# Kernel tuning notes

Measured on AMD Instinct MI355X. Metric: run time of the kernel, lower is better.

## Reference

```python
import jax, jax.numpy as jnp
import numpy as np

N = 50000      # nodes
E = 800000     # edges (avg degree 16)
IN, HID, OUT = 128, 128, 64


def setup_inputs() -> dict:
    key = jax.random.key(0)
    ks = jax.random.split(key, 6)
    x = jax.random.normal(ks[0], (N, IN), dtype=jnp.float32)
    edge_index = jax.random.randint(ks[1], (2, E), 0, N, dtype=jnp.int32)
    # GCNConv params (glorot-ish scaling)
    W1 = jax.random.normal(ks[2], (IN, HID), dtype=jnp.float32) * (1.0 / np.sqrt(IN))
    b1 = jnp.zeros((HID,), dtype=jnp.float32)
    W2 = jax.random.normal(ks[3], (HID, OUT), dtype=jnp.float32) * (1.0 / np.sqrt(HID))
    b2 = jnp.zeros((OUT,), dtype=jnp.float32)
    return {"x": x, "edge_index": edge_index, "W1": W1, "b1": b1, "W2": W2, "b2": b2}


def _gcn_conv(h, edge_index, W, b):
    """PyG GCNConv: linear transform, then sym-normalized aggregation with self-loops."""
    h = h @ W  # [N, out]
    src, dst = edge_index[0], edge_index[1]
    # degree including the added self-loop
    deg = jax.ops.segment_sum(jnp.ones((E,), h.dtype), dst, num_segments=N) + 1.0
    dinv = jax.lax.rsqrt(deg)                       # deg^{-1/2}
    norm = dinv[src] * dinv[dst]                    # [E]
    agg = jax.ops.segment_sum(h[src] * norm[:, None], dst, num_segments=N)
    agg = agg + h * (dinv * dinv)[:, None]          # self-loop term: deg^{-1} * h_i
    return agg + b


def reference(x, edge_index, W1, b1, W2, b2):
    h = jax.nn.relu(_gcn_conv(x, edge_index, W1, b1))
    h = jax.nn.relu(_gcn_conv(h, edge_index, W2, b2))
    return h
```

## Files before the change

### kernel.cpp

```cpp
#include <hip/hip_runtime.h>

#define DIN 128
#define DHID 128
#define DOUT 64
#define CAPB 6144
#define CHUNK 4096
#define EPT (CHUNK / 256)

typedef short bf16x8 __attribute__((ext_vector_type(8)));
typedef float f32x4 __attribute__((ext_vector_type(4)));

static __device__ __forceinline__ unsigned short f2bf(float f) {
  union { float f; unsigned u; } v; v.f = f;
  unsigned r = v.u + 0x7fffu + ((v.u >> 16) & 1u);
  return (unsigned short)(r >> 16);
}
static __device__ __forceinline__ float bf_lo(unsigned v) {
  union { unsigned u; float f; } t; t.u = v << 16; return t.f;
}
static __device__ __forceinline__ float bf_hi(unsigned v) {
  union { unsigned u; float f; } t; t.u = v & 0xffff0000u; return t.f;
}

static __device__ __forceinline__ void wcast_body(
    const float* __restrict__ W, unsigned short* __restrict__ Wf,
    int NOUT, int tid) {
  int f = tid >> 6;
  int lane = tid & 63;
  int t = f & 3;
  int nt = f >> 2;
  int kbase = t * 32 + (lane >> 4) * 8;
  int n = nt * 16 + (lane & 15);
#pragma unroll
  for (int j = 0; j < 8; ++j)
    Wf[(size_t)tid * 8 + j] = f2bf(W[(size_t)(kbase + j) * NOUT + n]);
}

__global__ __launch_bounds__(256) void init_kernel(
    const float* __restrict__ W1, const float* __restrict__ W2,
    unsigned short* __restrict__ Wf1, unsigned short* __restrict__ Wf2,
    int* __restrict__ bincursor) {
  const int b = blockIdx.x;
  const int t = threadIdx.x;
  if (b == 0) {
    bincursor[t] = 0;
  } else if (b <= 8) {
    wcast_body(W1, Wf1, DHID, (b - 1) * 256 + t);
  } else {
    wcast_body(W2, Wf2, DOUT, (b - 9) * 256 + t);
  }
}

static __device__ void gemm1_tile(
    const float* __restrict__ A, const unsigned short* __restrict__ Wf,
    unsigned short* __restrict__ C, int M, int tile) {
  constexpr int NT = DHID / 16;
  const int lane = threadIdx.x & 63;
  const int wave = threadIdx.x >> 6;
  const int g = lane >> 4;
  const int m15 = lane & 15;

  bf16x8 bfrag[NT * 4];
#pragma unroll
  for (int f = 0; f < NT * 4; ++f)
    bfrag[f] = *(const bf16x8*)(Wf + ((size_t)(f * 64 + lane)) * 8);

  const int rowbase = tile * 64 + wave * 16;
  if (rowbase >= M) return;
  f32x4 acc[NT];
#pragma unroll
  for (int nt = 0; nt < NT; ++nt) acc[nt] = (f32x4){0.f, 0.f, 0.f, 0.f};
  const float* arow = A + (size_t)(rowbase + m15) * 128 + g * 8;
  bf16x8 af[4];
#pragma unroll
  for (int t = 0; t < 4; ++t) {
    float4 a0 = *(const float4*)(arow + t * 32);
    float4 a1 = *(const float4*)(arow + t * 32 + 4);
    bf16x8 f;
    f[0] = (short)f2bf(a0.x); f[1] = (short)f2bf(a0.y);
    f[2] = (short)f2bf(a0.z); f[3] = (short)f2bf(a0.w);
    f[4] = (short)f2bf(a1.x); f[5] = (short)f2bf(a1.y);
    f[6] = (short)f2bf(a1.z); f[7] = (short)f2bf(a1.w);
    af[t] = f;
  }
#pragma unroll
  for (int t = 0; t < 4; ++t)
#pragma unroll
    for (int nt = 0; nt < NT; ++nt)
      acc[nt] = __builtin_amdgcn_mfma_f32_16x16x32_bf16(
          af[t], bfrag[nt * 4 + t], acc[nt], 0, 0, 0);
#pragma unroll
  for (int nt = 0; nt < NT; ++nt)
#pragma unroll
    for (int r = 0; r < 4; ++r) {
      int row = rowbase + g * 4 + r;
      if (row < M)
        C[(size_t)row * DHID + nt * 16 + m15] = f2bf(acc[nt][r]);
    }
}

__global__ __launch_bounds__(256) void phaseA_kernel(
    const int* __restrict__ src, const int* __restrict__ dst,
    int* __restrict__ bincursor, unsigned* __restrict__ binbuf, int E,
    int nbinA, const float* __restrict__ x,
    const unsigned short* __restrict__ Wf1, unsigned short* __restrict__ h1,
    int M) {
  __shared__ int hist[256];
  __shared__ int cnt[256];
  __shared__ int offs[256];
  __shared__ int cur[256];
  __shared__ int gbase[256];
  __shared__ unsigned stage[CHUNK];

  if ((int)blockIdx.x >= nbinA) {
    gemm1_tile(x, Wf1, h1, M, (int)blockIdx.x - nbinA);
    return;
  }

  const int t = threadIdx.x;
  const int base = blockIdx.x * CHUNK;
  const int n = min(CHUNK, E - base);

  hist[t] = 0;
  __syncthreads();

  unsigned rec[EPT];
  int rng[EPT];
#pragma unroll
  for (int j = 0; j < EPT; ++j) {
    int e = base + j * 256 + t;
    rng[j] = -1;
    if (e < E) {
      int d = dst[e];
      int s = src[e];
      int r = d >> 8;
      rng[j] = r;
      rec[j] = (unsigned)s | ((unsigned)(d & 255) << 16) | ((unsigned)r << 24);
      atomicAdd(&hist[r], 1);
    }
  }
  __syncthreads();
  int myc = hist[t];
  cnt[t] = myc;
  __syncthreads();
#pragma unroll
  for (int o = 1; o < 256; o <<= 1) {
    int u = (t >= o) ? hist[t - o] : 0;
    __syncthreads();
    hist[t] += u;
    __syncthreads();
  }
  offs[t] = hist[t] - myc;
  cur[t] = hist[t] - myc;
  __syncthreads();
#pragma unroll
  for (int j = 0; j < EPT; ++j) {
    if (rng[j] >= 0) {
      int pos = atomicAdd(&cur[rng[j]], 1);
      stage[pos] = rec[j];
    }
  }
  __syncthreads();
  int c = cnt[t];
  gbase[t] = c ? atomicAdd(&bincursor[t], c) : 0;
  __syncthreads();
  for (int i = t; i < n; i += 256) {
    unsigned v = stage[i];
    int r = v >> 24;
    int local = i - offs[r];
    int gpos = gbase[r] + local;
    if (gpos < CAPB) binbuf[(size_t)r * CAPB + gpos] = v & 0x00ffffffu;
  }
}

__global__ __launch_bounds__(256) void scan_local_kernel(
    const unsigned* __restrict__ binbuf, const int* __restrict__ bincursor,
    int* __restrict__ rowptr, int* __restrict__ bsum,
    float* __restrict__ dinv, int n) {
  __shared__ int deg[256];
  __shared__ int lds[256];
  const int t = threadIdx.x;
  const int b = blockIdx.x;
  deg[t] = 0;
  __syncthreads();
  const int cnt = min(bincursor[b], CAPB);
  const unsigned* seg = binbuf + (size_t)b * CAPB;
  for (int i = t; i < cnt; i += 256) atomicAdd(&deg[(seg[i] >> 16) & 0xff], 1);
  __syncthreads();
  const int i = b * 256 + t;
  int v = (i < n) ? deg[t] : 0;
  if (i < n) dinv[i] = rsqrtf((float)v + 1.0f);
  lds[t] = v;
  __syncthreads();
#pragma unroll
  for (int o = 1; o < 256; o <<= 1) {
    int u = (t >= o) ? lds[t - o] : 0;
    __syncthreads();
    lds[t] += u;
    __syncthreads();
  }
  if (i < n) rowptr[i] = lds[t] - v;
  if (t == 255) bsum[b] = lds[255];
}

__global__ __launch_bounds__(256) void binB_kernel(
    const unsigned* __restrict__ binbuf, const int* __restrict__ bincursor,
    int* __restrict__ rowptr, const int* __restrict__ bsum, int nr,
    const float* __restrict__ dinv, unsigned* __restrict__ recs, int n) {
  __shared__ int curs[256];
  __shared__ int bscan[256];
  __shared__ unsigned stage[CAPB];
  const int t = threadIdx.x;
  const int r = blockIdx.x;
  const int n0 = r * 256;
  const int nn = min(256, n - n0);

  int bv = (t < nr) ? bsum[t] : 0;
  bscan[t] = bv;
  __syncthreads();
#pragma unroll
  for (int o = 1; o < 256; o <<= 1) {
    int u = (t >= o) ? bscan[t - o] : 0;
    __syncthreads();
    bscan[t] += u;
    __syncthreads();
  }
  const int segbase = (r == 0) ? 0 : bscan[r - 1];

  if (t < nn) {
    int local = rowptr[n0 + t];
    curs[t] = local;
    rowptr[n0 + t] = local + segbase;
  }
  if (r == nr - 1 && t == 0) rowptr[n] = bscan[nr - 1];
  __syncthreads();
  const int cnt = min(bincursor[r], CAPB);
  const unsigned* seg = binbuf + (size_t)r * CAPB;
  for (int i = t; i < cnt; i += 256) {
    unsigned v = seg[i];
    int s = v & 0xffffu;
    int dl = (v >> 16) & 0xff;
    float w = dinv[s] * dinv[n0 + dl];
    int pos = atomicAdd(&curs[dl], 1);
    stage[pos] = (unsigned)s | ((unsigned)f2bf(w) << 16);
  }
  __syncthreads();
  for (int i = t; i < cnt; i += 256) recs[segbase + i] = stage[i];
}

__global__ __launch_bounds__(256) void agg1_gemm2_kernel(
    const unsigned short* __restrict__ h, const unsigned* __restrict__ recs,
    const int* __restrict__ rowptr, const float* __restrict__ dinv,
    const float* __restrict__ b1, const unsigned short* __restrict__ Wf2,
    unsigned short* __restrict__ h2, int n) {
  __shared__ unsigned short tile[16][136];
  const int wave = threadIdx.x >> 6;
  const int lane = threadIdx.x & 63;
  const int sub = lane >> 5;
  const int c = lane & 31;
  const int nbase = blockIdx.x * 16;
  const unsigned short* hc = h + c * 4;

  for (int q = 0; q < 4; ++q) {
    const int row = wave * 4 + q;
    const int nid = nbase + row;
    if (nid >= n) break;
    const float di = dinv[nid];
    const int p0 = rowptr[nid];
    const int end = rowptr[nid + 1];
    const int d = end - p0;
    float a0 = 0.f, a1 = 0.f, a2 = 0.f, a3 = 0.f;
    const int nb = (d + 15) >> 4;
    for (int b = 0; b < nb; ++b) {
      const int pb = p0 + (b << 4) + (sub << 3);
#pragma unroll
      for (int j = 0; j < 8; ++j) {
        int ei = pb + j;
        int ec = min(ei, end - 1);
        unsigned r = recs[ec];
        float w = (ei < end) ? bf_hi(r) : 0.f;
        const unsigned* vp = (const unsigned*)(hc + (size_t)(r & 0xffffu) * 128);
        unsigned u0 = vp[0];
        unsigned u1 = vp[1];
        a0 += bf_lo(u0) * w;
        a1 += bf_hi(u0) * w;
        a2 += bf_lo(u1) * w;
        a3 += bf_hi(u1) * w;
      }
    }
    a0 += __shfl_xor(a0, 32, 64);
    a1 += __shfl_xor(a1, 32, 64);
    a2 += __shfl_xor(a2, 32, 64);
    a3 += __shfl_xor(a3, 32, 64);
    if (sub == 0) {
      const unsigned* vp = (const unsigned*)(hc + (size_t)nid * 128);
      unsigned u0 = vp[0];
      unsigned u1 = vp[1];
      float w2 = di * di;
      a0 += bf_lo(u0) * w2;
      a1 += bf_hi(u0) * w2;
      a2 += bf_lo(u1) * w2;
      a3 += bf_hi(u1) * w2;
      float4 bv = *(const float4*)(b1 + c * 4);
      a0 = fmaxf(a0 + bv.x, 0.f);
      a1 = fmaxf(a1 + bv.y, 0.f);
      a2 = fmaxf(a2 + bv.z, 0.f);
      a3 = fmaxf(a3 + bv.w, 0.f);
      uint2 pk;
      pk.x = ((unsigned)f2bf(a1) << 16) | f2bf(a0);
      pk.y = ((unsigned)f2bf(a3) << 16) | f2bf(a2);
      *(uint2*)&tile[row][c * 4] = pk;
    }
  }
  __syncthreads();

  const int g = lane >> 4;
  const int m15 = lane & 15;
  f32x4 acc = (f32x4){0.f, 0.f, 0.f, 0.f};
#pragma unroll
  for (int t = 0; t < 4; ++t) {
    bf16x8 af = *(const bf16x8*)&tile[m15][t * 32 + g * 8];
    bf16x8 bf = *(const bf16x8*)(Wf2 + ((size_t)((wave * 4 + t) * 64 + lane)) * 8);
    acc = __builtin_amdgcn_mfma_f32_16x16x32_bf16(af, bf, acc, 0, 0, 0);
  }
#pragma unroll
  for (int r = 0; r < 4; ++r) {
    int row = nbase + g * 4 + r;
    if (row < n) h2[(size_t)row * DOUT + wave * 16 + m15] = f2bf(acc[r]);
  }
}

__global__ __launch_bounds__(256) void aggregate2_kernel(
    const unsigned short* __restrict__ h, const unsigned* __restrict__ recs,
    const int* __restrict__ rowptr, const float* __restrict__ dinv,
    const float* __restrict__ bias, float* __restrict__ out, int n) {
  const int wave = threadIdx.x >> 6;
  const int lane = threadIdx.x & 63;
  const int sub = lane >> 5;
  const int c = lane & 31;
  const int nid = blockIdx.x * 4 + wave;
  if (nid >= n) return;

  const float di = dinv[nid];
  const int p0 = rowptr[nid];
  const int end = rowptr[nid + 1];
  const int d = end - p0;
  const unsigned short* hc = h + c * 2;

  float a0 = 0.f, a1 = 0.f;
  const int nb = (d + 15) >> 4;
  for (int b = 0; b < nb; ++b) {
    const int pb = p0 + (b << 4) + (sub << 3);
#pragma unroll
    for (int j = 0; j < 8; ++j) {
      int ei = pb + j;
      int ec = min(ei, end - 1);
      unsigned r = recs[ec];
      float w = (ei < end) ? bf_hi(r) : 0.f;
      unsigned v = *(const unsigned*)(hc + (size_t)(r & 0xffffu) * 64);
      a0 += bf_lo(v) * w;
      a1 += bf_hi(v) * w;
    }
  }
  a0 += __shfl_xor(a0, 32, 64);
  a1 += __shfl_xor(a1, 32, 64);
  if (sub == 0) {
    unsigned v = *(const unsigned*)(hc + (size_t)nid * 64);
    float w2 = di * di;
    a0 += bf_lo(v) * w2;
    a1 += bf_hi(v) * w2;
    float2 bv = *(const float2*)(bias + c * 2);
    a0 = fmaxf(a0 + bv.x, 0.f);
    a1 = fmaxf(a1 + bv.y, 0.f);
    *(float2*)(out + (size_t)nid * 64 + c * 2) = make_float2(a0, a1);
  }
}

extern "C" void kernel_launch(void* const* d_in, const int* in_sizes, int n_in,
                              void* d_out, int out_size, void* d_ws, size_t ws_size,
                              hipStream_t stream) {
  const float* x = (const float*)d_in[0];
  const int* edge = (const int*)d_in[1];
  const float* W1 = (const float*)d_in[2];
  const float* b1 = (const float*)d_in[3];
  const float* W2 = (const float*)d_in[4];
  const float* b2 = (const float*)d_in[5];
  float* out = (float*)d_out;

  const int N = in_sizes[0] / DIN;
  const int E = in_sizes[1] / 2;
  const int* src = edge;
  const int* dst = edge + E;
  const int NR = (N + 255) >> 8;
  const int nbinA = (E + CHUNK - 1) / CHUNK;
  const int ntiles1 = (N + 63) / 64;

  char* base = (char*)d_ws;
  size_t off = 0;
  auto carve = [&](size_t bytes) {
    char* p = base + off;
    off += (bytes + 255) & ~(size_t)255;
    return p;
  };
  float* dinv = (float*)carve((size_t)N * 4);
  int* rowptr = (int*)carve((size_t)(N + 1) * 4);
  int* bsum = (int*)carve(256 * 4);
  int* bincursor = (int*)carve(256 * 4);
  unsigned* binbuf = (unsigned*)carve((size_t)NR * CAPB * 4 + CAPB * 4);
  unsigned* recs = (unsigned*)carve((size_t)E * 4);
  unsigned short* h1 = (unsigned short*)carve((size_t)N * DHID * 2);
  unsigned short* h2 = (unsigned short*)carve((size_t)N * DOUT * 2);
  unsigned short* Wf1 = (unsigned short*)carve((size_t)DIN * DHID * 2);
  unsigned short* Wf2 = (unsigned short*)carve((size_t)DHID * DOUT * 2);

  init_kernel<<<13, 256, 0, stream>>>(W1, W2, Wf1, Wf2, bincursor);
  phaseA_kernel<<<nbinA + ntiles1, 256, 0, stream>>>(
      src, dst, bincursor, binbuf, E, nbinA, x, Wf1, h1, N);
  scan_local_kernel<<<NR, 256, 0, stream>>>(binbuf, bincursor, rowptr, bsum, dinv, N);
  binB_kernel<<<NR, 256, 0, stream>>>(binbuf, bincursor, rowptr, bsum, NR, dinv, recs, N);
  agg1_gemm2_kernel<<<(N + 15) / 16, 256, 0, stream>>>(
      h1, recs, rowptr, dinv, b1, Wf2, h2, N);
  aggregate2_kernel<<<(N + 3) / 4, 256, 0, stream>>>(
      h2, recs, rowptr, dinv, b2, out, N);
}
```

Measured before the change: 168.8 us.

## Use per-bin local row ranges and wave-shuffled edge records in aggregation

```diff
diff --git a/kernel.cpp b/kernel.cpp
--- a/kernel.cpp
+++ b/kernel.cpp
@@ -175,8 +175,7 @@
 
 __global__ __launch_bounds__(256) void scan_local_kernel(
     const unsigned* __restrict__ binbuf, const int* __restrict__ bincursor,
-    int* __restrict__ rowptr, int* __restrict__ bsum,
-    float* __restrict__ dinv, int n) {
+    int2* __restrict__ rowrange, float* __restrict__ dinv, int n) {
   __shared__ int deg[256];
   __shared__ int lds[256];
   const int t = threadIdx.x;
@@ -188,7 +187,7 @@
   for (int i = t; i < cnt; i += 256) atomicAdd(&deg[(seg[i] >> 16) & 0xff], 1);
   __syncthreads();
   const int i = b * 256 + t;
-  int v = (i < n) ? deg[t] : 0;
+  int v = deg[t];
   if (i < n) dinv[i] = rsqrtf((float)v + 1.0f);
   lds[t] = v;
   __syncthreads();
@@ -199,40 +198,19 @@
     lds[t] += u;
     __syncthreads();
   }
-  if (i < n) rowptr[i] = lds[t] - v;
-  if (t == 255) bsum[b] = lds[255];
+  if (i < n) rowrange[i] = make_int2(lds[t] - v, lds[t]);
 }
 
 __global__ __launch_bounds__(256) void binB_kernel(
     const unsigned* __restrict__ binbuf, const int* __restrict__ bincursor,
-    int* __restrict__ rowptr, const int* __restrict__ bsum, int nr,
-    const float* __restrict__ dinv, unsigned* __restrict__ recs, int n) {
+    const int2* __restrict__ rowrange, const float* __restrict__ dinv,
+    unsigned* __restrict__ recs, int n) {
   __shared__ int curs[256];
-  __shared__ int bscan[256];
   __shared__ unsigned stage[CAPB];
   const int t = threadIdx.x;
   const int r = blockIdx.x;
   const int n0 = r * 256;
-  const int nn = min(256, n - n0);
-
-  int bv = (t < nr) ? bsum[t] : 0;
-  bscan[t] = bv;
-  __syncthreads();
-#pragma unroll
-  for (int o = 1; o < 256; o <<= 1) {
-    int u = (t >= o) ? bscan[t - o] : 0;
-    __syncthreads();
-    bscan[t] += u;
-    __syncthreads();
-  }
-  const int segbase = (r == 0) ? 0 : bscan[r - 1];
-
-  if (t < nn) {
-    int local = rowptr[n0 + t];
-    curs[t] = local;
-    rowptr[n0 + t] = local + segbase;
-  }
-  if (r == nr - 1 && t == 0) rowptr[n] = bscan[nr - 1];
+  curs[t] = (n0 + t < n) ? rowrange[n0 + t].x : 0;
   __syncthreads();
   const int cnt = min(bincursor[r], CAPB);
   const unsigned* seg = binbuf + (size_t)r * CAPB;
@@ -245,12 +223,13 @@
     stage[pos] = (unsigned)s | ((unsigned)f2bf(w) << 16);
   }
   __syncthreads();
-  for (int i = t; i < cnt; i += 256) recs[segbase + i] = stage[i];
+  unsigned* rout = recs + (size_t)r * CAPB;
+  for (int i = t; i < cnt; i += 256) rout[i] = stage[i];
 }
 
 __global__ __launch_bounds__(256) void agg1_gemm2_kernel(
     const unsigned short* __restrict__ h, const unsigned* __restrict__ recs,
-    const int* __restrict__ rowptr, const float* __restrict__ dinv,
+    const int2* __restrict__ rowrange, const float* __restrict__ dinv,
     const float* __restrict__ b1, const unsigned short* __restrict__ Wf2,
     unsigned short* __restrict__ h2, int n) {
   __shared__ unsigned short tile[16][136];
@@ -259,34 +238,54 @@
   const int sub = lane >> 5;
   const int c = lane & 31;
   const int nbase = blockIdx.x * 16;
+  const unsigned* rbase = recs + (size_t)(nbase >> 8) * CAPB;
   const unsigned short* hc = h + c * 4;
+
+  int np0[4], npe[4];
+  unsigned wrec[4];
+#pragma unroll
+  for (int q = 0; q < 4; ++q) {
+    int nid = nbase + wave * 4 + q;
+    int2 rr = (nid < n) ? rowrange[nid] : make_int2(0, 0);
+    np0[q] = rr.x;
+    npe[q] = rr.y;
+    int last = (rr.y > rr.x) ? (rr.y - 1) : rr.x;
+    wrec[q] = rbase[min(rr.x + lane, last)];
+  }
 
   for (int q = 0; q < 4; ++q) {
     const int row = wave * 4 + q;
     const int nid = nbase + row;
     if (nid >= n) break;
     const float di = dinv[nid];
-    const int p0 = rowptr[nid];
-    const int end = rowptr[nid + 1];
-    const int d = end - p0;
     float a0 = 0.f, a1 = 0.f, a2 = 0.f, a3 = 0.f;
-    const int nb = (d + 15) >> 4;
-    for (int b = 0; b < nb; ++b) {
-      const int pb = p0 + (b << 4) + (sub << 3);
-#pragma unroll
-      for (int j = 0; j < 8; ++j) {
-        int ei = pb + j;
-        int ec = min(ei, end - 1);
-        unsigned r = recs[ec];
-        float w = (ei < end) ? bf_hi(r) : 0.f;
-        const unsigned* vp = (const unsigned*)(hc + (size_t)(r & 0xffffu) * 128);
-        unsigned u0 = vp[0];
-        unsigned u1 = vp[1];
-        a0 += bf_lo(u0) * w;
-        a1 += bf_hi(u0) * w;
-        a2 += bf_lo(u1) * w;
-        a3 += bf_hi(u1) * w;
+    unsigned mw = wrec[q];
+    int p = np0[q];
+    const int end = npe[q];
+    while (true) {
+      const int dw = min(64, end - p);
+      const int nb = (dw + 15) >> 4;
+      for (int b = 0; b < nb; ++b) {
+#pragma unroll
+        for (int j = 0; j < 8; ++j) {
+          int ei = b * 16 + sub * 8 + j;
+          unsigned r = __shfl(mw, ei, 64);
+          if (ei < dw) {
+            float w = bf_hi(r);
+            const unsigned* vp =
+                (const unsigned*)(hc + (size_t)(r & 0xffffu) * 128);
+            unsigned u0 = vp[0];
+            unsigned u1 = vp[1];
+            a0 += bf_lo(u0) * w;
+            a1 += bf_hi(u0) * w;
+            a2 += bf_lo(u1) * w;
+            a3 += bf_hi(u1) * w;
+          }
+        }
       }
+      p += 64;
+      if (p >= end) break;
+      mw = rbase[min(p + lane, end - 1)];
     }
     a0 += __shfl_xor(a0, 32, 64);
     a1 += __shfl_xor(a1, 32, 64);
@@ -332,7 +331,7 @@
 
 __global__ __launch_bounds__(256) void aggregate2_kernel(
     const unsigned short* __restrict__ h, const unsigned* __restrict__ recs,
-    const int* __restrict__ rowptr, const float* __restrict__ dinv,
+    const int2* __restrict__ rowrange, const float* __restrict__ dinv,
     const float* __restrict__ bias, float* __restrict__ out, int n) {
   const int wave = threadIdx.x >> 6;
   const int lane = threadIdx.x & 63;
@@ -341,26 +340,35 @@
   const int nid = blockIdx.x * 4 + wave;
   if (nid >= n) return;
 
+  const unsigned* rbase = recs + (size_t)(nid >> 8) * CAPB;
   const float di = dinv[nid];
-  const int p0 = rowptr[nid];
-  const int end = rowptr[nid + 1];
-  const int d = end - p0;
+  int2 rr = rowrange[nid];
+  int p = rr.x;
+  const int end = rr.y;
+  const int last = (end > p) ? (end - 1) : p;
   const unsigned short* hc = h + c * 2;
 
+  unsigned mw = rbase[min(p + lane, last)];
   float a0 = 0.f, a1 = 0.f;
-  const int nb = (d + 15) >> 4;
-  for (int b = 0; b < nb; ++b) {
-    const int pb = p0 + (b << 4) + (sub << 3);
-#pragma unroll
-    for (int j = 0; j < 8; ++j) {
-      int ei = pb + j;
-      int ec = min(ei, end - 1);
-      unsigned r = recs[ec];
-      float w = (ei < end) ? bf_hi(r) : 0.f;
-      unsigned v = *(const unsigned*)(hc + (size_t)(r & 0xffffu) * 64);
-      a0 += bf_lo(v) * w;
-      a1 += bf_hi(v) * w;
-    }
+  while (true) {
+    const int dw = min(64, end - p);
+    const int nb = (dw + 15) >> 4;
+    for (int b = 0; b < nb; ++b) {
+#pragma unroll
+      for (int j = 0; j < 8; ++j) {
+        int ei = b * 16 + sub * 8 + j;
+        unsigned r = __shfl(mw, ei, 64);
+        if (ei < dw) {
+          float w = bf_hi(r);
+          unsigned v = *(const unsigned*)(hc + (size_t)(r & 0xffffu) * 64);
+          a0 += bf_lo(v) * w;
+          a1 += bf_hi(v) * w;
+        }
+      }
+    }
+    p += 64;
+    if (p >= end) break;
+    mw = rbase[min(p + lane, end - 1)];
   }
   a0 += __shfl_xor(a0, 32, 64);
   a1 += __shfl_xor(a1, 32, 64);
@@ -403,11 +411,10 @@
     return p;
   };
   float* dinv = (float*)carve((size_t)N * 4);
-  int* rowptr = (int*)carve((size_t)(N + 1) * 4);
-  int* bsum = (int*)carve(256 * 4);
+  int2* rowrange = (int2*)carve((size_t)N * 8);
   int* bincursor = (int*)carve(256 * 4);
   unsigned* binbuf = (unsigned*)carve((size_t)NR * CAPB * 4 + CAPB * 4);
-  unsigned* recs = (unsigned*)carve((size_t)E * 4);
+  unsigned* recs = (unsigned*)carve((size_t)NR * CAPB * 4 + 1024);
   unsigned short* h1 = (unsigned short*)carve((size_t)N * DHID * 2);
   unsigned short* h2 = (unsigned short*)carve((size_t)N * DOUT * 2);
   unsigned short* Wf1 = (unsigned short*)carve((size_t)DIN * DHID * 2);
@@ -416,10 +423,10 @@
   init_kernel<<<13, 256, 0, stream>>>(W1, W2, Wf1, Wf2, bincursor);
   phaseA_kernel<<<nbinA + ntiles1, 256, 0, stream>>>(
       src, dst, bincursor, binbuf, E, nbinA, x, Wf1, h1, N);
-  scan_local_kernel<<<NR, 256, 0, stream>>>(binbuf, bincursor, rowptr, bsum, dinv, N);
-  binB_kernel<<<NR, 256, 0, stream>>>(binbuf, bincursor, rowptr, bsum, NR, dinv, recs, N);
+  scan_local_kernel<<<NR, 256, 0, stream>>>(binbuf, bincursor, rowrange, dinv, N);
+  binB_kernel<<<NR, 256, 0, stream>>>(binbuf, bincursor, rowrange, dinv, recs, N);
   agg1_gemm2_kernel<<<(N + 15) / 16, 256, 0, stream>>>(
-      h1, recs, rowptr, dinv, b1, Wf2, h2, N);
+      h1, recs, rowrange, dinv, b1, Wf2, h2, N);
   aggregate2_kernel<<<(N + 3) / 4, 256, 0, stream>>>(
-      h2, recs, rowptr, dinv, b2, out, N);
-}
+      h2, recs, rowrange, dinv, b2, out, N);
+}
```

Measured after the change: 195.5 us. +15.9%, slower.
